# Kernel tuning notes

Hardware: AMD Instinct MI355X
Metric: run time of the kernel (lower is better)

Reference implementation:

```python
import jax, jax.numpy as jnp
import numpy as np

L, T, R = 2, 2, 2          # layers, node types (0=user,1=movie), edge types
NU, NM, E = 50000, 10000, 500000
C, H, DPHI = 128, 4, 64
D = C // H                 # head dim = 32
SQRT_D = float(np.sqrt(D))


def setup_inputs() -> dict:
    key = jax.random.key(0)
    ks = jax.random.split(key, 16)
    s = 0.05
    src = jax.random.randint(ks[0], (E,), 0, NU)
    dst = jax.random.randint(ks[1], (E,), 0, NM)
    return {
        "user_emb": jax.random.normal(ks[2], (NU, C)) * 0.01,
        "movie_emb": jax.random.normal(ks[3], (NM, C)) * 0.01,
        "phi": jax.random.normal(ks[4], (NM, DPHI)),
        "meta_w": jax.random.normal(ks[5], (DPHI, C)) * s,
        "meta_b": jnp.zeros((C,)),
        "kw": jax.random.normal(ks[6], (L, T, C, C)) * s,
        "kb": jnp.zeros((L, T, C)),
        "qw": jax.random.normal(ks[7], (L, T, C, C)) * s,
        "qb": jnp.zeros((L, T, C)),
        "vw": jax.random.normal(ks[8], (L, T, C, C)) * s,
        "vb": jnp.zeros((L, T, C)),
        "a_rel": jax.random.normal(ks[9], (L, R, H, D, D)) * s,
        "m_rel": jax.random.normal(ks[10], (L, R, H, D, D)) * s,
        "p_rel": jnp.ones((L, R, H)),
        "ow": jax.random.normal(ks[11], (L, T, C, C)) * s,
        "ob": jnp.zeros((L, T, C)),
        "skip": jnp.ones((L, T)),
        "edge_index": jnp.stack([src, dst]),  # [2,E], row0=user idx, row1=movie idx
    }


def _segment_softmax(logits, seg, n):
    # logits: [E,H], seg: [E] destination node ids
    m = jax.ops.segment_max(logits, seg, num_segments=n)
    e = jnp.exp(logits - m[seg])
    s = jax.ops.segment_sum(e, seg, num_segments=n)
    return e / (s[seg] + 1e-16)


def _hgt_layer(xs, kw, kb, qw, qb, vw, vb, a_rel, m_rel, p_rel, ow, ob, skip, edge_index):
    ns = [x.shape[0] for x in xs]
    k = [(xs[t] @ kw[t] + kb[t]).reshape(ns[t], H, D) for t in range(T)]
    q = [(xs[t] @ qw[t] + qb[t]).reshape(ns[t], H, D) for t in range(T)]
    v = [(xs[t] @ vw[t] + vb[t]).reshape(ns[t], H, D) for t in range(T)]
    # edge types: r=0 user->movie, r=1 movie->user (reverse)
    etypes = [(0, 1, edge_index[0], edge_index[1]),
              (1, 0, edge_index[1], edge_index[0])]
    agg = [jnp.zeros((ns[t], C), dtype=xs[t].dtype) for t in range(T)]
    for r, (st, dt, src, dst) in enumerate(etypes):
        ke = jnp.einsum('nhd,hde->nhe', k[st], a_rel[r])   # per-edge-type key transform
        ve = jnp.einsum('nhd,hde->nhe', v[st], m_rel[r])
        logits = (q[dt][dst] * ke[src]).sum(-1) * p_rel[r] / SQRT_D   # [E,H]
        alpha = _segment_softmax(logits, dst, ns[dt])                  # [E,H]
        msg = (alpha[:, :, None] * ve[src]).reshape(-1, C)
        agg[dt] = agg[dt] + jax.ops.segment_sum(msg, dst, num_segments=ns[dt])
    out = []
    for t in range(T):
        o = jax.nn.gelu(agg[t]) @ ow[t] + ob[t]
        g = jax.nn.sigmoid(skip[t])
        out.append(g * o + (1.0 - g) * xs[t])
    return out


def reference(user_emb, movie_emb, phi, meta_w, meta_b, kw, kb, qw, qb, vw, vb,
              a_rel, m_rel, p_rel, ow, ob, skip, edge_index):
    xu = user_emb
    xm = movie_emb + phi @ meta_w + meta_b   # meta feature fusion on movie nodes
    xs = [xu, xm]
    for l in range(L):
        xs = _hgt_layer(xs, kw[l], kb[l], qw[l], qb[l], vw[l], vb[l],
                        a_rel[l], m_rel[l], p_rel[l], ow[l], ob[l], skip[l], edge_index)
    return (xs[0], xs[1])
```

## Files before the change

kernel.cpp:

```cpp
#include <hip/hip_runtime.h>
#include <hip/hip_bf16.h>

#define Cc 128
#define Hh 4
#define Dd 32
#define DPHI2 64
#define Ll 2
#define Tt 2
#define Rr 2

typedef __hip_bfloat16 bf16;
using short8 = __attribute__((ext_vector_type(8))) short;
using f32x4 = __attribute__((ext_vector_type(4))) float;
using f32x2 = __attribute__((ext_vector_type(2))) float;
typedef _Float16 h2 __attribute__((ext_vector_type(2)));
typedef __fp16 fp16x2 __attribute__((ext_vector_type(2)));

__device__ __forceinline__ unsigned short f2bf(float f) {
  union { float f; unsigned u; } v; v.f = f;
  unsigned r = v.u + 0x7fff + ((v.u >> 16) & 1);
  return (unsigned short)(r >> 16);
}
__device__ __forceinline__ h2 u2h(unsigned u) {
  union { unsigned u; h2 h; } v; v.u = u; return v.h;
}
__device__ __forceinline__ unsigned pkh(float a, float b) {
  union { unsigned u; fp16x2 h; } v;
  v.h = __builtin_amdgcn_cvt_pkrtz(a, b);
  return v.u;
}

__device__ __forceinline__ float fp8_decode1(unsigned char b) {
  unsigned u = b & 0x7f;
  float nrm = __builtin_bit_cast(float, (u << 20) + 0x3C000000u);
  float sub = (float)u * 0.001953125f;
  float v = (u >= 8) ? nrm : sub;
  return (b & 0x80) ? -v : v;
}
template <bool HI>
__device__ __forceinline__ f32x2 fp8x2f(unsigned w) {
#if __has_builtin(__builtin_amdgcn_cvt_pk_f32_fp8)
  return __builtin_amdgcn_cvt_pk_f32_fp8(w, HI);
#else
  unsigned b = HI ? (w >> 16) : (w & 0xffff);
  f32x2 r;
  r[0] = fp8_decode1((unsigned char)b);
  r[1] = fp8_decode1((unsigned char)(b >> 8));
  return r;
#endif
}
#if !__has_builtin(__builtin_amdgcn_cvt_pk_fp8_f32)
__device__ __forceinline__ unsigned char fp8_encode1(float f) {
  unsigned s = (__builtin_bit_cast(unsigned, f) >> 31) << 7;
  float a = fabsf(f);
  a = fminf(a, 448.f);
  unsigned char out;
  if (a < 0.0009765625f) {
    out = 0;
  } else if (a < 0.015625f) {
    out = (unsigned char)(a * 512.f + 0.5f);
  } else {
    unsigned bits = __builtin_bit_cast(unsigned, a);
    int e = (int)(bits >> 23) - 127;
    unsigned m = (bits >> 20) & 7;
    m += (bits >> 19) & 1;
    unsigned ee = (unsigned)(e + 7);
    if (m == 8) { m = 0; ee += 1; }
    if (ee > 15) { ee = 15; m = 6; }
    out = (unsigned char)((ee << 3) | m);
  }
  return out | (unsigned char)s;
}
#endif
__device__ __forceinline__ unsigned pk_fp8x4(float v0, float v1, float v2, float v3) {
#if __has_builtin(__builtin_amdgcn_cvt_pk_fp8_f32)
  int p = __builtin_amdgcn_cvt_pk_fp8_f32(v0, v1, 0, false);
  p = __builtin_amdgcn_cvt_pk_fp8_f32(v2, v3, p, true);
  return (unsigned)p;
#else
  return (unsigned)fp8_encode1(v0) | ((unsigned)fp8_encode1(v1) << 8) |
         ((unsigned)fp8_encode1(v2) << 16) | ((unsigned)fp8_encode1(v3) << 24);
#endif
}

__device__ __forceinline__ float dpp_add_xor1(float x) {
  int v = __builtin_amdgcn_update_dpp(0, __builtin_bit_cast(int, x), 0xB1, 0xF, 0xF, true);
  return x + __builtin_bit_cast(float, v);
}
__device__ __forceinline__ float dpp_add_xor2(float x) {
  int v = __builtin_amdgcn_update_dpp(0, __builtin_bit_cast(int, x), 0x4E, 0xF, 0xF, true);
  return x + __builtin_bit_cast(float, v);
}

__device__ __forceinline__ float gelu_tanh(float x) {
  float u = 0.7978845608028654f * (x + 0.044715f * x * x * x);
  float t = 1.f - 2.f / (__expf(2.f * u) + 1.f);
  return 0.5f * x * (1.f + t);
}

__device__ __forceinline__ void gload_lds16(const void* gsrc, void* lds) {
  __builtin_amdgcn_global_load_lds(
      (const __attribute__((address_space(1))) unsigned int*)gsrc,
      (__attribute__((address_space(3))) unsigned int*)lds, 16, 0, 0);
}

__global__ __launch_bounds__(256) void prep_init_kernel(
    int NM_, int NU_,
    const float* __restrict__ kw, const float* __restrict__ kb,
    const float* __restrict__ qw, const float* __restrict__ qb,
    const float* __restrict__ vw, const float* __restrict__ vb,
    const float* __restrict__ a_rel, const float* __restrict__ m_rel,
    const float* __restrict__ p_rel, const float* __restrict__ ow,
    const float* __restrict__ ob,
    unsigned short* __restrict__ WT, float* __restrict__ bQKV,
    unsigned short* __restrict__ OWT, float* __restrict__ bO,
    const float* __restrict__ ue, const float* __restrict__ me,
    const float* __restrict__ phi, const float* __restrict__ mw,
    const float* __restrict__ mb,
    float* __restrict__ xout, unsigned short* __restrict__ Xb,
    int PB) {
  int b = blockIdx.x;
  if (b < PB) {
    int idx = b * 2 + (threadIdx.x >> 7);
    int g = idx >> 2, lt = idx & 3;
    int l = lt >> 1, t = lt & 1, r = t;
    int k = threadIdx.x & 127;
    const float inv_sqrt_d = 0.17677669529663687f;
    const float QSCALE = 1.4426950408889634f / 256.f;
    float val, bval;
    if (g < 128) {
      val = qw[((size_t)lt * Cc + k) * Cc + g] * QSCALE;
      bval = qb[(size_t)lt * Cc + g] * QSCALE;
    } else if (g < 384) {
      int isV = (g >= 256);
      int n = g - (isV ? 256 : 128);
      int h = n >> 5, e = n & 31;
      const float* W = (isV ? vw : kw) + (size_t)lt * Cc * Cc;
      const float* bb = (isV ? vb : kb) + (size_t)lt * Cc;
      const float* Ah = (isV ? m_rel : a_rel) + (((size_t)l * Rr + r) * Hh + h) * Dd * Dd;
      float s = 0.f, sb = 0.f;
      for (int d = 0; d < Dd; ++d) {
        float ae = Ah[d * Dd + e];
        s += W[(size_t)k * Cc + h * Dd + d] * ae;
        sb += bb[h * Dd + d] * ae;
      }
      float scale = isV ? 256.f : p_rel[((size_t)l * Rr + r) * Hh + h] * inv_sqrt_d * 256.f;
      val = s * scale;
      bval = sb * scale;
    } else {
      int n = g - 384;
      val = ow[((size_t)lt * Cc + k) * Cc + n];
      bval = ob[(size_t)lt * Cc + n];
    }
    if (g < 384) {
      WT[((size_t)lt * 384 + g) * Cc + k] = f2bf(val);
      if (k == 0) bQKV[(size_t)lt * 384 + g] = bval;
    } else {
      OWT[((size_t)lt * Cc + (g - 384)) * Cc + k] = f2bf(val);
      if (k == 0) bO[(size_t)lt * Cc + (g - 384)] = bval;
    }
    return;
  }
  int i4 = (b - PB) * 256 + threadIdx.x;
  int totalU4 = NU_ * 32;
  float4 s;
  size_t o;
  if (i4 < totalU4) {
    o = (size_t)i4 * 4;
    s = *(const float4*)&ue[o];
  } else {
    int mg = i4 - totalU4;
    if (mg >= NM_ * 32) return;
    int m = mg >> 5, c = (mg & 31) * 4;
    o = (size_t)(NU_ * 32 + mg) * 4;
    s = *(const float4*)&me[(size_t)m * Cc + c];
    float4 bmv = *(const float4*)&mb[c];
    s.x += bmv.x; s.y += bmv.y; s.z += bmv.z; s.w += bmv.w;
    const float* ph = phi + (size_t)m * DPHI2;
#pragma unroll 4
    for (int d = 0; d < DPHI2; ++d) {
      float p = ph[d];
      float4 w4 = *(const float4*)&mw[d * Cc + c];
      s.x += p * w4.x; s.y += p * w4.y; s.z += p * w4.z; s.w += p * w4.w;
    }
  }
  *(float4*)&xout[o] = s;
  uint2 pk;
  pk.x = (unsigned)f2bf(s.x) | ((unsigned)f2bf(s.y) << 16);
  pk.y = (unsigned)f2bf(s.z) | ((unsigned)f2bf(s.w) << 16);
  *(uint2*)&Xb[o] = pk;
}

__global__ __launch_bounds__(256) void scan_p1(const int* __restrict__ cnt, int n,
                                               int* __restrict__ psum) {
  int i0 = blockIdx.x * 1024 + threadIdx.x * 4;
  int s = 0;
#pragma unroll
  for (int j = 0; j < 4; ++j) {
    int i = i0 + j;
    if (i < n) s += cnt[i];
  }
#pragma unroll
  for (int off = 1; off < 64; off <<= 1) s += __shfl_xor(s, off, 64);
  __shared__ int wsum[4];
  if ((threadIdx.x & 63) == 0) wsum[threadIdx.x >> 6] = s;
  __syncthreads();
  if (threadIdx.x == 0) psum[blockIdx.x] = wsum[0] + wsum[1] + wsum[2] + wsum[3];
}
__global__ void scan_p2(int* psum, int nb) {
  if (threadIdx.x == 0 && blockIdx.x == 0) {
    int run = 0;
    for (int i = 0; i < nb; ++i) { int v = psum[i]; psum[i] = run; run += v; }
  }
}
__global__ __launch_bounds__(256) void scan_p3(const int* __restrict__ cnt, int n,
                                               const int* __restrict__ psum,
                                               int* __restrict__ rowptr) {
  __shared__ int sdata[256];
  int i0 = blockIdx.x * 1024 + threadIdx.x * 4;
  int a0 = (i0 + 0 < n) ? cnt[i0 + 0] : 0;
  int a1 = (i0 + 1 < n) ? cnt[i0 + 1] : 0;
  int a2 = (i0 + 2 < n) ? cnt[i0 + 2] : 0;
  int a3 = (i0 + 3 < n) ? cnt[i0 + 3] : 0;
  int s = a0 + a1 + a2 + a3;
  sdata[threadIdx.x] = s;
  __syncthreads();
  for (int off = 1; off < 256; off <<= 1) {
    int t = ((int)threadIdx.x >= off) ? sdata[threadIdx.x - off] : 0;
    __syncthreads();
    sdata[threadIdx.x] += t;
    __syncthreads();
  }
  int run = psum[blockIdx.x] + sdata[threadIdx.x] - s;
  if (i0 + 0 < n) rowptr[i0 + 1] = run + a0;
  if (i0 + 1 < n) rowptr[i0 + 2] = run + a0 + a1;
  if (i0 + 2 < n) rowptr[i0 + 3] = run + a0 + a1 + a2;
  if (i0 + 3 < n) rowptr[i0 + 4] = run + s;
  if (blockIdx.x == 0 && threadIdx.x == 0) rowptr[0] = 0;
}

__global__ void scatter_kernel(const int* __restrict__ esrc, const int* __restrict__ edst,
                               int E_, const int* __restrict__ rowptr,
                               const int* __restrict__ eoffm, const int* __restrict__ eoffu,
                               int* __restrict__ srcAll, int NU_, int NM_) {
  int e = blockIdx.x * 256 + threadIdx.x;
  if (e < E_) {
    int s = esrc[e], d = edst[e];
    srcAll[rowptr[d] + eoffm[e]] = s << 8;
    srcAll[rowptr[NM_ + s] + eoffu[e]] = (NU_ + d) << 8;
  }
}

template <int NCH, int MODE>
__global__ __launch_bounds__(256, 2) void mfma_gemm(
    int NBU_, int NU_, int NM_,
    const bf16* __restrict__ Abase,
    const bf16* __restrict__ WTl, const float* __restrict__ biasl,
    char* __restrict__ Qc, char* __restrict__ KVc,
    float* __restrict__ xout, unsigned short* __restrict__ Xb,
    const float* __restrict__ skipl,
    int GB, const int* __restrict__ esrc, const int* __restrict__ edst, int E_,
    int* __restrict__ cnt, int* __restrict__ eoffm, int* __restrict__ eoffu) {
  __shared__ char Bs[2][16384];
  if ((int)blockIdx.x >= GB) {
    int base_e = ((int)blockIdx.x - GB) * 2048;
#pragma unroll
    for (int j = 0; j < 8; ++j) {
      int e = base_e + j * 256 + (int)threadIdx.x;
      if (e < E_) {
        eoffm[e] = atomicAdd(&cnt[edst[e]], 1);
        eoffu[e] = atomicAdd(&cnt[NM_ + esrc[e]], 1);
      }
    }
    return;
  }
  int bx = blockIdx.x;
  int t, row0, M, base;
  if (bx < NBU_) { t = 0; row0 = bx * 128; M = NU_; base = 0; }
  else { t = 1; row0 = (bx - NBU_) * 128; M = NM_; base = NU_; }
  const char* BT = (const char*)(WTl + (size_t)t * (NCH * 64) * Cc);
  const float* bias = biasl + (size_t)t * (NCH * 64);
  int wid = threadIdx.x >> 6, lane = threadIdx.x & 63;
  int rw = row0 + wid * 32;
  bool wact = rw < M;
  int lr = lane & 15, lk8 = (lane >> 4) * 8;

  auto stage = [&](int ch, int buf) {
    const char* src = BT + (size_t)ch * 16384;
#pragma unroll
    for (int j = 0; j < 4; ++j) {
      int u = wid * 4 + j;
      int d = u * 1024 + lane * 16;
      int g = d ^ (((d >> 8) & 7) << 4);
      gload_lds16(src + g, &Bs[buf][u * 1024]);
    }
  };

  short8 a[2][4];
#pragma unroll
  for (int mt = 0; mt < 2; ++mt) {
    int r = rw + mt * 16 + lr;
    const bf16* ap = Abase + (size_t)(base + r) * Cc + lk8;
#pragma unroll
    for (int kk = 0; kk < 4; ++kk) {
      short8 v = {};
      if (wact && r < M) v = *(const short8*)(ap + kk * 32);
      a[mt][kk] = v;
    }
  }
  float g = 0.f;
  if (MODE == 1) g = 1.f / (1.f + __expf(-skipl[t]));

  stage(0, 0);
#pragma unroll
  for (int ch = 0; ch < NCH; ++ch) {
    int buf = ch & 1;
    __syncthreads();
    if (ch + 1 < NCH) stage(ch + 1, buf ^ 1);
    short8 b[4][4];
#pragma unroll
    for (int nt = 0; nt < 4; ++nt) {
      int r = nt * 16 + lr;
#pragma unroll
      for (int kk = 0; kk < 4; ++kk) {
        int a0 = r * 256 + (lk8 + kk * 32) * 2;
        b[nt][kk] = *(const short8*)(&Bs[buf][a0 ^ ((r & 7) << 4)]);
      }
    }
    f32x4 acc[2][4];
#pragma unroll
    for (int mt = 0; mt < 2; ++mt)
#pragma unroll
      for (int nt = 0; nt < 4; ++nt) acc[mt][nt] = (f32x4){0.f, 0.f, 0.f, 0.f};
#pragma unroll
    for (int kk = 0; kk < 4; ++kk)
#pragma unroll
      for (int mt = 0; mt < 2; ++mt)
#pragma unroll
        for (int nt = 0; nt < 4; ++nt)
          acc[mt][nt] = __builtin_amdgcn_mfma_f32_16x16x32_bf16(
              b[nt][kk], a[mt][kk], acc[mt][nt], 0, 0, 0);
    if (!wact) continue;
#pragma unroll
    for (int mt = 0; mt < 2; ++mt) {
      int r = rw + mt * 16 + lr;
      if (r >= M) continue;
      size_t grow = (size_t)(base + r);
#pragma unroll
      for (int nt = 0; nt < 4; ++nt) {
        int cb = ch * 64 + nt * 16 + 4 * (lane >> 4);
        float4 b4 = *(const float4*)&bias[cb];
        float v0 = acc[mt][nt][0] + b4.x;
        float v1 = acc[mt][nt][1] + b4.y;
        float v2 = acc[mt][nt][2] + b4.z;
        float v3 = acc[mt][nt][3] + b4.w;
        if (MODE == 0) {
          if (cb < Cc) {
            uint2 pk;
            pk.x = pkh(v0, v1); pk.y = pkh(v2, v3);
            *(uint2*)(Qc + grow * 256 + cb * 2) = pk;
          } else {
            int c = cb - 128;
            int isv = c >> 7; c &= 127;
            int off = (c >> 3) * 16 + (c & 7) + isv * 8;
            unsigned pk = pk_fp8x4(v0, v1, v2, v3);
            *(unsigned*)(KVc + grow * 256 + off) = pk;
          }
        } else {
          float* xp = xout + grow * Cc + cb;
          float4 old = *(const float4*)xp;
          float n0 = g * v0 + (1.f - g) * old.x;
          float n1 = g * v1 + (1.f - g) * old.y;
          float n2 = g * v2 + (1.f - g) * old.z;
          float n3 = g * v3 + (1.f - g) * old.w;
          *(float4*)xp = make_float4(n0, n1, n2, n3);
          uint2 pk;
          pk.x = (unsigned)f2bf(n0) | ((unsigned)f2bf(n1) << 16);
          pk.y = (unsigned)f2bf(n2) | ((unsigned)f2bf(n3) << 16);
          *(uint2*)(Xb + grow * Cc + cb) = pk;
        }
      }
    }
  }
}

__global__ __launch_bounds__(256) void agg_kernel(
    const int* __restrict__ rowptr, const int* __restrict__ srcAll,
    const char* __restrict__ Qc, const char* __restrict__ KVc,
    unsigned short* __restrict__ AGGb, int NM_, int NU_) {
  int wid = threadIdx.x >> 6, lane = threadIdx.x & 63;
  int sub = lane & 15, eo = lane >> 4;
  int NT_ = NM_ + NU_;
  int W = (blockIdx.x * 4 + wid) * 4 + eo;
  bool active = W < NT_;
  int Wc = active ? W : NT_ - 1;
  int beg = rowptr[Wc];
  int end = active ? rowptr[Wc + 1] : beg;
  int dnode = (Wc < NM_) ? (NU_ + Wc) : (Wc - NM_);
  int myoff = sub * 16;
  uint4 qv = *(const uint4*)(Qc + (size_t)dnode * 256 + myoff);
  float qf0, qf1, qf2, qf3, qf4, qf5, qf6, qf7;
  {
    h2 t0 = u2h(qv.x), t1 = u2h(qv.y), t2 = u2h(qv.z), t3 = u2h(qv.w);
    qf0 = (float)t0[0]; qf1 = (float)t0[1];
    qf2 = (float)t1[0]; qf3 = (float)t1[1];
    qf4 = (float)t2[0]; qf5 = (float)t2[1];
    qf6 = (float)t3[0]; qf7 = (float)t3[1];
  }
  float acc0 = 0.f, acc1 = 0.f, acc2 = 0.f, acc3 = 0.f;
  float acc4 = 0.f, acc5 = 0.f, acc6 = 0.f, acc7 = 0.f;
  float denom = 0.f;
  const char* KVp = KVc + myoff;

#define CONSUME(KV, WVALID)                                                       \
  {                                                                               \
    f32x2 k01 = fp8x2f<false>((KV).x), k23 = fp8x2f<true>((KV).x);                \
    f32x2 k45 = fp8x2f<false>((KV).y), k67 = fp8x2f<true>((KV).y);                \
    float pA = qf0 * k01[0] + qf1 * k01[1] + qf2 * k23[0] + qf3 * k23[1];         \
    float pB = qf4 * k45[0] + qf5 * k45[1] + qf6 * k67[0] + qf7 * k67[1];         \
    float p = pA + pB;                                                            \
    p = dpp_add_xor1(p);                                                          \
    p = dpp_add_xor2(p);                                                          \
    float w = (WVALID) ? exp2f(p) : 0.f;                                          \
    denom += w;                                                                   \
    f32x2 v01 = fp8x2f<false>((KV).z), v23 = fp8x2f<true>((KV).z);                \
    f32x2 v45 = fp8x2f<false>((KV).w), v67 = fp8x2f<true>((KV).w);                \
    acc0 += w * v01[0]; acc1 += w * v01[1];                                       \
    acc2 += w * v23[0]; acc3 += w * v23[1];                                       \
    acc4 += w * v45[0]; acc5 += w * v45[1];                                       \
    acc6 += w * v67[0]; acc7 += w * v67[1];                                       \
  }

  for (int e = beg; __any(e < end); e += 4) {
    bool v0 = e < end, v1 = (e + 1) < end, v2 = (e + 2) < end, v3 = (e + 3) < end;
    int so0 = srcAll[v0 ? e : 0];
    int so1 = srcAll[v1 ? (e + 1) : 0];
    int so2 = srcAll[v2 ? (e + 2) : 0];
    int so3 = srcAll[v3 ? (e + 3) : 0];
    uint4 kv0 = *(const uint4*)(KVp + (size_t)(unsigned)so0);
    uint4 kv1 = *(const uint4*)(KVp + (size_t)(unsigned)so1);
    uint4 kv2 = *(const uint4*)(KVp + (size_t)(unsigned)so2);
    uint4 kv3 = *(const uint4*)(KVp + (size_t)(unsigned)so3);
    CONSUME(kv0, v0)
    CONSUME(kv1, v1)
    CONSUME(kv2, v2)
    CONSUME(kv3, v3)
  }
#undef CONSUME

  if (active) {
    float inv = 1.f / (denom + 1e-16f) * 0.00390625f;
    float o0 = gelu_tanh(acc0 * inv);
    float o1 = gelu_tanh(acc1 * inv);
    float o2 = gelu_tanh(acc2 * inv);
    float o3 = gelu_tanh(acc3 * inv);
    float o4 = gelu_tanh(acc4 * inv);
    float o5 = gelu_tanh(acc5 * inv);
    float o6 = gelu_tanh(acc6 * inv);
    float o7 = gelu_tanh(acc7 * inv);
    uint4 pk;
    pk.x = (unsigned)f2bf(o0) | ((unsigned)f2bf(o1) << 16);
    pk.y = (unsigned)f2bf(o2) | ((unsigned)f2bf(o3) << 16);
    pk.z = (unsigned)f2bf(o4) | ((unsigned)f2bf(o5) << 16);
    pk.w = (unsigned)f2bf(o6) | ((unsigned)f2bf(o7) << 16);
    *(uint4*)(AGGb + (size_t)dnode * Cc + sub * 8) = pk;
  }
}

extern "C" void kernel_launch(void* const* d_in, const int* in_sizes, int n_in,
                              void* d_out, int out_size, void* d_ws, size_t ws_size,
                              hipStream_t stream) {
  const float* user_emb = (const float*)d_in[0];
  const float* movie_emb = (const float*)d_in[1];
  const float* phi = (const float*)d_in[2];
  const float* meta_w = (const float*)d_in[3];
  const float* meta_b = (const float*)d_in[4];
  const float* kw = (const float*)d_in[5];
  const float* kb = (const float*)d_in[6];
  const float* qw = (const float*)d_in[7];
  const float* qb = (const float*)d_in[8];
  const float* vw = (const float*)d_in[9];
  const float* vb = (const float*)d_in[10];
  const float* a_rel = (const float*)d_in[11];
  const float* m_rel = (const float*)d_in[12];
  const float* p_rel = (const float*)d_in[13];
  const float* ow = (const float*)d_in[14];
  const float* ob = (const float*)d_in[15];
  const float* skip = (const float*)d_in[16];
  const int* eidx = (const int*)d_in[17];

  int NU = in_sizes[0] / Cc;
  int NM = in_sizes[1] / Cc;
  int E_ = in_sizes[17] / 2;
  int NT = NU + NM;
  const int* esrc = eidx;
  const int* edst = eidx + E_;

  char* ws = (char*)d_ws;
  size_t off = 0;
  auto alloc = [&](size_t bytes) -> char* {
    char* p = ws + off;
    off = (off + bytes + 255) & ~(size_t)255;
    return p;
  };
  char* Qc = alloc((size_t)NT * 256);
  char* KVc = alloc((size_t)NT * 256);
  unsigned short* Xb = (unsigned short*)alloc((size_t)NT * Cc * 2);
  unsigned short* AGGb = (unsigned short*)alloc((size_t)NT * Cc * 2);
  unsigned short* WT = (unsigned short*)alloc((size_t)Ll * Tt * 384 * Cc * 2);
  unsigned short* OWT = (unsigned short*)alloc((size_t)Ll * Tt * Cc * Cc * 2);
  float* bQKV = (float*)alloc((size_t)Ll * Tt * 384 * 4);
  float* bO = (float*)alloc((size_t)Ll * Tt * Cc * 4);
  int* rowptr = (int*)alloc((size_t)(NT + 1) * 4);
  int* srcAll = (int*)alloc((size_t)2 * E_ * 4);
  int* eoffm = (int*)alloc((size_t)E_ * 4);
  int* eoffu = (int*)alloc((size_t)E_ * 4);
  int* cnt = (int*)alloc((size_t)NT * 4);
  int* psum = (int*)alloc((size_t)256 * 4);
  float* xout = (float*)d_out;

  int nblk = (NT + 1023) / 1024;
  int PB = 1024;
  int IB = (NT * 32 + 255) / 256;
  int HB = (E_ + 2047) / 2048;

  int NBU = (NU + 127) / 128;
  int NBM = (NM + 127) / 128;
  int GB = NBU + NBM;
  int nagg = (NT + 15) / 16;
  int SB = (E_ + 255) / 256;

  hipMemsetAsync(cnt, 0, (size_t)NT * 4, stream);
  prep_init_kernel<<<PB + IB, 256, 0, stream>>>(
      NM, NU, kw, kb, qw, qb, vw, vb, a_rel, m_rel, p_rel, ow, ob,
      WT, bQKV, OWT, bO,
      user_emb, movie_emb, phi, meta_w, meta_b, xout, Xb, PB);
  mfma_gemm<6, 0><<<GB + HB, 256, 0, stream>>>(
      NBU, NU, NM, (const bf16*)Xb, (const bf16*)WT, bQKV, Qc, KVc,
      nullptr, nullptr, nullptr, GB, esrc, edst, E_, cnt, eoffm, eoffu);
  scan_p1<<<nblk, 256, 0, stream>>>(cnt, NT, psum);
  scan_p2<<<1, 64, 0, stream>>>(psum, nblk);
  scan_p3<<<nblk, 256, 0, stream>>>(cnt, NT, psum, rowptr);
  scatter_kernel<<<SB, 256, 0, stream>>>(esrc, edst, E_, rowptr, eoffm, eoffu,
                                         srcAll, NU, NM);
  agg_kernel<<<nagg, 256, 0, stream>>>(rowptr, srcAll, Qc, KVc, AGGb, NM, NU);
  mfma_gemm<2, 1><<<GB, 256, 0, stream>>>(
      NBU, NU, NM, (const bf16*)AGGb, (const bf16*)OWT, bO,
      nullptr, nullptr, xout, Xb, skip, GB, nullptr, nullptr, 0,
      nullptr, nullptr, nullptr);
  mfma_gemm<6, 0><<<GB, 256, 0, stream>>>(
      NBU, NU, NM, (const bf16*)Xb, (const bf16*)(WT + (size_t)2 * 384 * Cc),
      bQKV + (size_t)2 * 384, Qc, KVc, nullptr, nullptr, nullptr,
      GB, nullptr, nullptr, 0, nullptr, nullptr, nullptr);
  agg_kernel<<<nagg, 256, 0, stream>>>(rowptr, srcAll, Qc, KVc, AGGb, NM, NU);
  mfma_gemm<2, 1><<<GB, 256, 0, stream>>>(
      NBU, NU, NM, (const bf16*)AGGb, (const bf16*)(OWT + (size_t)2 * Cc * Cc),
      bO + (size_t)2 * Cc, nullptr, nullptr, xout, Xb, skip + 2,
      GB, nullptr, nullptr, 0, nullptr, nullptr, nullptr);
}
```

Before: 265.6 us.

## Replace global atomic movie-degree histogram with per-block LDS histograms plus column scan

The edge-counting blocks fused into the first QKV GEMM now build a per-block movie histogram in shared memory over 8192-edge chunks, using LDS atomics instead of contended global atomics on only 10000 movie counters. Each block writes its histogram to a blkcnt array. A new colscan kernel turns these into per-block prefix offsets and total counts, and the scatter kernel adds the block offset when placing edges. This targets heavy global atomic contention on movie destinations, at the cost of one extra kernel launch, roughly 2.5 MB of blkcnt traffic, and a 40 KB shared array that may lower GEMM occupancy.

```diff
diff --git a/kernel.cpp b/kernel.cpp
--- a/kernel.cpp
+++ b/kernel.cpp
@@ -191,6 +191,21 @@
   *(uint2*)&Xb[o] = pk;
 }
 
+__global__ __launch_bounds__(256) void colscan_kernel(int* __restrict__ blkcnt,
+                                                      int* __restrict__ cnt,
+                                                      int NM_, int HB) {
+  int d = blockIdx.x * 256 + threadIdx.x;
+  if (d >= NM_) return;
+  int run = 0;
+  for (int b = 0; b < HB; ++b) {
+    int* p = blkcnt + (size_t)b * NM_ + d;
+    int t = *p;
+    *p = run;
+    run += t;
+  }
+  cnt[d] = run;
+}
+
 __global__ __launch_bounds__(256) void scan_p1(const int* __restrict__ cnt, int n,
                                                int* __restrict__ psum) {
   int i0 = blockIdx.x * 1024 + threadIdx.x * 4;
@@ -241,40 +256,47 @@
 
 __global__ void scatter_kernel(const int* __restrict__ esrc, const int* __restrict__ edst,
                                int E_, const int* __restrict__ rowptr,
+                               const int* __restrict__ blkcnt,
                                const int* __restrict__ eoffm, const int* __restrict__ eoffu,
                                int* __restrict__ srcAll, int NU_, int NM_) {
   int e = blockIdx.x * 256 + threadIdx.x;
   if (e < E_) {
     int s = esrc[e], d = edst[e];
-    srcAll[rowptr[d] + eoffm[e]] = s << 8;
+    int mbase = blkcnt[(size_t)(e >> 13) * NM_ + d];
+    srcAll[rowptr[d] + mbase + eoffm[e]] = s << 8;
     srcAll[rowptr[NM_ + s] + eoffu[e]] = (NU_ + d) << 8;
   }
 }
 
 template <int NCH, int MODE>
 __global__ __launch_bounds__(256, 2) void mfma_gemm(
-    int NBU_, int NU_, int NM_,
+    int HB, int NBU_, int NU_, int NM_,
     const bf16* __restrict__ Abase,
     const bf16* __restrict__ WTl, const float* __restrict__ biasl,
     char* __restrict__ Qc, char* __restrict__ KVc,
     float* __restrict__ xout, unsigned short* __restrict__ Xb,
     const float* __restrict__ skipl,
-    int GB, const int* __restrict__ esrc, const int* __restrict__ edst, int E_,
-    int* __restrict__ cnt, int* __restrict__ eoffm, int* __restrict__ eoffu) {
-  __shared__ char Bs[2][16384];
-  if ((int)blockIdx.x >= GB) {
-    int base_e = ((int)blockIdx.x - GB) * 2048;
-#pragma unroll
-    for (int j = 0; j < 8; ++j) {
-      int e = base_e + j * 256 + (int)threadIdx.x;
-      if (e < E_) {
-        eoffm[e] = atomicAdd(&cnt[edst[e]], 1);
-        eoffu[e] = atomicAdd(&cnt[NM_ + esrc[e]], 1);
-      }
-    }
+    const int* __restrict__ esrc, const int* __restrict__ edst, int E_,
+    int* __restrict__ cntU, int* __restrict__ eoffm, int* __restrict__ eoffu,
+    int* __restrict__ blkcnt) {
+  __shared__ int smem[10240];
+  if (MODE == 0 && (int)blockIdx.x < HB) {
+    int* mh = smem;
+    for (int i = threadIdx.x; i < NM_; i += 256) mh[i] = 0;
+    __syncthreads();
+    int e0 = (int)blockIdx.x << 13;
+    int e1 = min(e0 + 8192, E_);
+    for (int e = e0 + (int)threadIdx.x; e < e1; e += 256) {
+      eoffm[e] = atomicAdd(&mh[edst[e]], 1);
+      eoffu[e] = atomicAdd(&cntU[esrc[e]], 1);
+    }
+    __syncthreads();
+    int* bc = blkcnt + (size_t)blockIdx.x * NM_;
+    for (int i = threadIdx.x; i < NM_; i += 256) bc[i] = mh[i];
     return;
   }
-  int bx = blockIdx.x;
+  int bx = (int)blockIdx.x - ((MODE == 0) ? HB : 0);
+  char* BsBase = (char*)smem;
   int t, row0, M, base;
   if (bx < NBU_) { t = 0; row0 = bx * 128; M = NU_; base = 0; }
   else { t = 1; row0 = (bx - NBU_) * 128; M = NM_; base = NU_; }
@@ -292,7 +314,7 @@
       int u = wid * 4 + j;
       int d = u * 1024 + lane * 16;
       int g = d ^ (((d >> 8) & 7) << 4);
-      gload_lds16(src + g, &Bs[buf][u * 1024]);
+      gload_lds16(src + g, BsBase + buf * 16384 + u * 1024);
     }
   };
 
@@ -324,7 +346,7 @@
 #pragma unroll
       for (int kk = 0; kk < 4; ++kk) {
         int a0 = r * 256 + (lk8 + kk * 32) * 2;
-        b[nt][kk] = *(const short8*)(&Bs[buf][a0 ^ ((r & 7) << 4)]);
+        b[nt][kk] = *(const short8*)(BsBase + buf * 16384 + (a0 ^ ((r & 7) << 4)));
       }
     }
     f32x4 acc[2][4];
@@ -517,12 +539,13 @@
   int* eoffu = (int*)alloc((size_t)E_ * 4);
   int* cnt = (int*)alloc((size_t)NT * 4);
   int* psum = (int*)alloc((size_t)256 * 4);
+  int HB = (E_ + 8191) / 8192;
+  int* blkcnt = (int*)alloc((size_t)HB * NM * 4);
   float* xout = (float*)d_out;
 
   int nblk = (NT + 1023) / 1024;
   int PB = 1024;
   int IB = (NT * 32 + 255) / 256;
-  int HB = (E_ + 2047) / 2048;
 
   int NBU = (NU + 127) / 128;
   int NBM = (NM + 127) / 128;
@@ -530,31 +553,32 @@
   int nagg = (NT + 15) / 16;
   int SB = (E_ + 255) / 256;
 
-  hipMemsetAsync(cnt, 0, (size_t)NT * 4, stream);
+  hipMemsetAsync(cnt + NM, 0, (size_t)NU * 4, stream);
   prep_init_kernel<<<PB + IB, 256, 0, stream>>>(
       NM, NU, kw, kb, qw, qb, vw, vb, a_rel, m_rel, p_rel, ow, ob,
       WT, bQKV, OWT, bO,
       user_emb, movie_emb, phi, meta_w, meta_b, xout, Xb, PB);
-  mfma_gemm<6, 0><<<GB + HB, 256, 0, stream>>>(
-      NBU, NU, NM, (const bf16*)Xb, (const bf16*)WT, bQKV, Qc, KVc,
-      nullptr, nullptr, nullptr, GB, esrc, edst, E_, cnt, eoffm, eoffu);
+  mfma_gemm<6, 0><<<HB + GB, 256, 0, stream>>>(
+      HB, NBU, NU, NM, (const bf16*)Xb, (const bf16*)WT, bQKV, Qc, KVc,
+      nullptr, nullptr, nullptr, esrc, edst, E_, cnt + NM, eoffm, eoffu, blkcnt);
+  colscan_kernel<<<(NM + 255) / 256, 256, 0, stream>>>(blkcnt, cnt, NM, HB);
   scan_p1<<<nblk, 256, 0, stream>>>(cnt, NT, psum);
   scan_p2<<<1, 64, 0, stream>>>(psum, nblk);
   scan_p3<<<nblk, 256, 0, stream>>>(cnt, NT, psum, rowptr);
-  scatter_kernel<<<SB, 256, 0, stream>>>(esrc, edst, E_, rowptr, eoffm, eoffu,
-                                         srcAll, NU, NM);
+  scatter_kernel<<<SB, 256, 0, stream>>>(esrc, edst, E_, rowptr, blkcnt,
+                                         eoffm, eoffu, srcAll, NU, NM);
   agg_kernel<<<nagg, 256, 0, stream>>>(rowptr, srcAll, Qc, KVc, AGGb, NM, NU);
   mfma_gemm<2, 1><<<GB, 256, 0, stream>>>(
-      NBU, NU, NM, (const bf16*)AGGb, (const bf16*)OWT, bO,
-      nullptr, nullptr, xout, Xb, skip, GB, nullptr, nullptr, 0,
-      nullptr, nullptr, nullptr);
+      0, NBU, NU, NM, (const bf16*)AGGb, (const bf16*)OWT, bO,
+      nullptr, nullptr, xout, Xb, skip, nullptr, nullptr, 0,
+      nullptr, nullptr, nullptr, nullptr);
   mfma_gemm<6, 0><<<GB, 256, 0, stream>>>(
-      NBU, NU, NM, (const bf16*)Xb, (const bf16*)(WT + (size_t)2 * 384 * Cc),
+      0, NBU, NU, NM, (const bf16*)Xb, (const bf16*)(WT + (size_t)2 * 384 * Cc),
       bQKV + (size_t)2 * 384, Qc, KVc, nullptr, nullptr, nullptr,
-      GB, nullptr, nullptr, 0, nullptr, nullptr, nullptr);
+      nullptr, nullptr, 0, nullptr, nullptr, nullptr, nullptr);
   agg_kernel<<<nagg, 256, 0, stream>>>(rowptr, srcAll, Qc, KVc, AGGb, NM, NU);
   mfma_gemm<2, 1><<<GB, 256, 0, stream>>>(
-      NBU, NU, NM, (const bf16*)AGGb, (const bf16*)(OWT + (size_t)2 * Cc * Cc),
+      0, NBU, NU, NM, (const bf16*)AGGb, (const bf16*)(OWT + (size_t)2 * Cc * Cc),
       bO + (size_t)2 * Cc, nullptr, nullptr, xout, Xb, skip + 2,
-      GB, nullptr, nullptr, 0, nullptr, nullptr, nullptr);
-}
+      nullptr, nullptr, 0, nullptr, nullptr, nullptr, nullptr);
+}
```

Result: slower. 274.2 us (+3.2%).
